# Performance work log

Hardware: AMD Instinct MI355X
Metric: run time of the kernel (lower is better)

The kernel has to match this reference:

```python
import jax, jax.numpy as jnp
import numpy as np

EMBED = 1024
HEADS = 16
HEAD_DIM = EMBED // HEADS
DIVIDER = int(np.sqrt(HEAD_DIM))  # torch code uses int(sqrt(head_dim)) == 8


def setup_inputs() -> dict:
    key = jax.random.key(0)
    ks = jax.random.split(key, 9)
    B, S = 2, 2048
    scale = 1.0 / np.sqrt(EMBED)
    def lin(kw, kb):
        W = jax.random.uniform(kw, (EMBED, EMBED), jnp.float32, -scale, scale)
        b = jax.random.uniform(kb, (EMBED,), jnp.float32, -scale, scale)
        return W, b
    Wq, bq = lin(ks[0], ks[1])
    Wk, bk = lin(ks[2], ks[3])
    Wv, bv = lin(ks[4], ks[5])
    Wo, bo = lin(ks[6], ks[7])
    x = jax.random.normal(ks[8], (B, S, EMBED), jnp.float32)
    return {"x": x, "Wq": Wq, "bq": bq, "Wk": Wk, "bk": bk,
            "Wv": Wv, "bv": bv, "Wo": Wo, "bo": bo}


def reference(x, Wq, bq, Wk, bk, Wv, bv, Wo, bo):
    B, S, _ = x.shape
    # projections (torch Linear: x @ W.T + b)
    q = x @ Wq.T + bq
    k = x @ Wk.T + bk
    v = x @ Wv.T + bv
    # split heads: [B, S, H, D] -> [B, H, S, D]
    def heads(t):
        return t.reshape(B, S, HEADS, HEAD_DIM).transpose(0, 2, 1, 3)
    q, k, v = heads(q), heads(k), heads(v)
    # scores [B, H, S, S]
    scores = jnp.einsum('bhsd,bhtd->bhst', q, k) / DIVIDER
    attn = jax.nn.softmax(scores, axis=-1)
    out = jnp.einsum('bhst,bhtd->bhsd', attn, v)
    out = out.transpose(0, 2, 1, 3).reshape(B, S, EMBED)
    return out @ Wo.T + bo
```

## Files before the change

### kernel.cpp

```cpp
#include <hip/hip_runtime.h>
#include <hip/hip_bf16.h>
#include <stdint.h>

using bf16 = __hip_bfloat16;
typedef __attribute__((ext_vector_type(8))) short   short8;
typedef __attribute__((ext_vector_type(4))) float   floatx4;
typedef __attribute__((ext_vector_type(2))) unsigned int uint2v;

static __device__ __forceinline__ unsigned short f2bf(float f) {
    return __builtin_bit_cast(unsigned short, __float2bfloat16(f));
}

static __device__ __forceinline__ uint4 load8bf(const void* p, size_t e, int f) {
    if (!f) return *(const uint4*)((const ushort*)p + e);
    const float* fp = (const float*)p + e;
    float4 a = *(const float4*)fp;
    float4 b = *(const float4*)(fp + 4);
    union { uint4 u; unsigned short s[8]; } r;
    r.s[0] = f2bf(a.x); r.s[1] = f2bf(a.y); r.s[2] = f2bf(a.z); r.s[3] = f2bf(a.w);
    r.s[4] = f2bf(b.x); r.s[5] = f2bf(b.y); r.s[6] = f2bf(b.z); r.s[7] = f2bf(b.w);
    return r.u;
}
static __device__ __forceinline__ float loadScalar(const void* p, int i, int f) {
    return f ? ((const float*)p)[i] : __bfloat162float(((const bf16*)p)[i]);
}

#define GLL16(g, l)                                                          \
    __builtin_amdgcn_global_load_lds(                                        \
        (const __attribute__((address_space(1))) void*)(g),                  \
        (__attribute__((address_space(3))) void*)(l), 16, 0, 0)

__global__ void detect_dtype(const ushort* __restrict__ x, int* __restrict__ flag) {
    __shared__ int cnt;
    if (threadIdx.x == 0) cnt = 0;
    __syncthreads();
    unsigned short u = x[threadIdx.x * 2];
    int e = (u >> 7) & 0xFF;
    int bad = (e > 133 || e < 94) ? 1 : 0;
    atomicAdd(&cnt, bad);
    __syncthreads();
    if (threadIdx.x == 0) *flag = (cnt > 64) ? 1 : 0;
}

__global__ void cvt_bf16(const void* __restrict__ x,  const void* __restrict__ Wq,
                         const void* __restrict__ Wk, const void* __restrict__ Wv,
                         const void* __restrict__ Wo,
                         ushort* __restrict__ out, const int* __restrict__ flagp)
{
    const int f = *flagp;
    const size_t M1 = (size_t)1 << 20, M4 = (size_t)4 << 20;
    size_t i = ((size_t)blockIdx.x * 256 + threadIdx.x) * 8;
    const void* src; size_t off;
    if (i < M4)            { src = x;  off = i; }
    else if (i < M4 + M1)  { src = Wq; off = i - M4; }
    else if (i < M4 + 2*M1){ src = Wk; off = i - (M4 + M1); }
    else if (i < M4 + 3*M1){ src = Wv; off = i - (M4 + 2*M1); }
    else                   { src = Wo; off = i - (M4 + 3*M1); }
    *(uint4*)(out + i) = load8bf(src, off, f);
}

__global__ __launch_bounds__(512, 4)
void gemm_dual(const ushort* __restrict__ A,
               const ushort* __restrict__ Wa, const ushort* __restrict__ Wb2,
               const void* __restrict__ Ba, const void* __restrict__ Bb,
               void* __restrict__ Oa, void* __restrict__ Ob_,
               int pa, int pb, int nb_off, int out_ext,
               const int* __restrict__ flagp)
{
    __shared__ ushort pool[32768];

    const int f  = *flagp;
    const int m0 = blockIdx.x * 128;
    const int n0a = blockIdx.y * 64;
    const int n0b = n0a + nb_off;
    const int tid  = threadIdx.x;
    const int lane = tid & 63;
    const int wave = tid >> 6;
    const int wm   = wave & 3;
    const int wn   = wave >> 2;
    const int r15  = lane & 15;
    const int quad = lane >> 4;

    const int   my_pm = wn ? pb : pa;
    const void* my_Bi = wn ? Bb : Ba;
    void*       my_O  = wn ? Ob_ : Oa;
    const int   my_n0 = wn ? n0b : n0a;

    const int l8 = lane >> 3, s8 = lane & 7;
    const int ar0 = wave * 16 + l8;
    const int ar1 = ar0 + 8;
    const int wr0 = wave * 16 + l8;
    const int wr1 = wr0 + 8;
    const ushort* gA0 = A + (size_t)(m0 + ar0) * 1024 + ((s8 ^ (ar0 & 7)) << 3);
    const ushort* gA1 = A + (size_t)(m0 + ar1) * 1024 + ((s8 ^ (ar1 & 7)) << 3);
    const ushort* gW0 = (wr0 < 64 ? Wa + (size_t)(n0a + wr0) * 1024
                                  : Wb2 + (size_t)(n0b + wr0 - 64) * 1024)
                        + ((s8 ^ (wr0 & 7)) << 3);
    const ushort* gW1 = (wr1 < 64 ? Wa + (size_t)(n0a + wr1) * 1024
                                  : Wb2 + (size_t)(n0b + wr1 - 64) * 1024)
                        + ((s8 ^ (wr1 & 7)) << 3);

    floatx4 acc[2][4];
#pragma unroll
    for (int mb = 0; mb < 2; mb++)
#pragma unroll
        for (int db = 0; db < 4; db++) acc[mb][db] = (floatx4){0.f, 0.f, 0.f, 0.f};

    GLL16(gA0, pool + wave * 1024);
    GLL16(gA1, pool + wave * 1024 + 512);
    GLL16(gW0, pool + 16384 + wave * 1024);
    GLL16(gW1, pool + 16384 + wave * 1024 + 512);

    for (int kb = 0; kb < 1024; kb += 64) {
        const int cur = (kb >> 6) & 1;
        ushort* xs  = pool + cur * 8192;
        ushort* wsm = pool + 16384 + cur * 8192;
        if (kb + 64 < 1024) {
            ushort* xn = pool + (cur ^ 1) * 8192;
            ushort* wn_ = pool + 16384 + (cur ^ 1) * 8192;
            GLL16(gA0 + kb + 64, xn + wave * 1024);
            GLL16(gA1 + kb + 64, xn + wave * 1024 + 512);
            GLL16(gW0 + kb + 64, wn_ + wave * 1024);
            GLL16(gW1 + kb + 64, wn_ + wave * 1024 + 512);
            asm volatile("s_waitcnt vmcnt(4)" ::: "memory");
        } else {
            asm volatile("s_waitcnt vmcnt(0)" ::: "memory");
        }
        __builtin_amdgcn_s_barrier();
        __builtin_amdgcn_sched_barrier(0);
#pragma unroll
        for (int ks = 0; ks < 2; ks++) {
            short8 af[2];
#pragma unroll
            for (int mb = 0; mb < 2; mb++) {
                int arow = wm * 32 + mb * 16 + r15;
                af[mb] = *(const short8*)(
                    &xs[arow * 64 + (((ks * 4 + quad) ^ (arow & 7)) << 3)]);
            }
#pragma unroll
            for (int db = 0; db < 4; db++) {
                int brow = wn * 64 + db * 16 + r15;
                short8 bv = *(const short8*)(
                    &wsm[brow * 64 + (((ks * 4 + quad) ^ (brow & 7)) << 3)]);
#pragma unroll
                for (int mb = 0; mb < 2; mb++)
                    acc[mb][db] = __builtin_amdgcn_mfma_f32_16x16x32_bf16(
                        af[mb], bv, acc[mb][db], 0, 0, 0);
            }
        }
        __builtin_amdgcn_s_barrier();
    }

    if (my_pm == 2) {
#pragma unroll
        for (int mb = 0; mb < 2; mb++)
#pragma unroll
            for (int db = 0; db < 4; db++) {
                int d = db * 16 + r15;
                float bias = loadScalar(my_Bi, my_n0 + d, f);
                int s4 = wm * 32 + mb * 16 + quad * 4;
                union { uint2 u; ushort us[4]; } pk;
#pragma unroll
                for (int r = 0; r < 4; r++) pk.us[r] = f2bf(acc[mb][db][r] + bias);
                *(uint2*)(&pool[d * 128 + (((s4 >> 3) ^ (d & 15)) << 3) + (s4 & 7)])
                    = pk.u;
            }
    } else {
#pragma unroll
        for (int mb = 0; mb < 2; mb++)
#pragma unroll
            for (int db = 0; db < 4; db++) {
                int col = my_n0 + db * 16 + r15;
                float bias = loadScalar(my_Bi, col, f);
#pragma unroll
                for (int r = 0; r < 4; r++) {
                    int row = m0 + wm * 32 + mb * 16 + quad * 4 + r;
                    float v = acc[mb][db][r] + bias;
                    if (my_pm == 1) {
                        int hh = col >> 6, d = col & 63;
                        int b_ = row >> 11, s = row & 2047;
                        ((ushort*)my_O)[(((size_t)(b_ * 16 + hh) * 2048 + s) << 6) + d]
                            = f2bf(v);
                    } else if (out_ext && f) {
                        ((float*)my_O)[(size_t)row * 1024 + col] = v;
                    } else {
                        ((ushort*)my_O)[(size_t)row * 1024 + col] = f2bf(v);
                    }
                }
            }
    }

    if (pa == 2 || pb == 2) {
        __syncthreads();
        void* OutT = (pb == 2) ? Ob_ : Oa;
        const int nT  = (pb == 2) ? n0b : n0a;
        const int b_  = m0 >> 11;
        const int h   = nT >> 6;
        const int sl0 = m0 & 2047;
#pragma unroll
        for (int rr = 0; rr < 2; rr++) {
            int idx = rr * 512 + tid;
            int d = idx >> 4, sgrp = idx & 15;
            uint4 v = *(const uint4*)(&pool[d * 128 + ((sgrp ^ (d & 15)) << 3)]);
            *(uint4*)((ushort*)OutT +
                      ((size_t)((b_ * 16 + h) * 64 + d) << 11) + sl0 + sgrp * 8) = v;
        }
    }
}

template<int BM>
__global__ __launch_bounds__(512, 4)
void gemm_bt(const void* __restrict__ A,
             const void* __restrict__ Wa, const void* __restrict__ Wb,
             const void* __restrict__ Ba, const void* __restrict__ Bb,
             void* __restrict__ Oa, void* __restrict__ Ob_,
             int pa, int pb, int a_ext, int out_ext,
             const int* __restrict__ flagp)
{
    constexpr int MB = BM / 128;
    constexpr int P  = BM / 64;
    constexpr int SG = BM / 8;
    __shared__ ushort pool[BM * 64 + 4096];

    const int f  = *flagp;
    const int fA = a_ext ? f : 0;
    const int z  = blockIdx.z;
    const void* W   = z ? Wb : Wa;
    const void* Bi  = z ? Bb : Ba;
    void*       Out = z ? Ob_ : Oa;
    const int   pm  = z ? pb : pa;

    const int m0 = blockIdx.x * BM;
    const int n0 = blockIdx.y * 64;
    const int tid  = threadIdx.x;
    const int lane = tid & 63;
    const int wave = tid >> 6;
    const int r15  = lane & 15;
    const int quad = lane >> 4;

    const int srow = tid >> 3;
    const int sg   = tid & 7;

    ushort* xs  = pool;
    ushort* wsm = pool + BM * 64;

    floatx4 acc[MB][4];
#pragma unroll
    for (int mb = 0; mb < MB; mb++)
#pragma unroll
        for (int db = 0; db < 4; db++) acc[mb][db] = (floatx4){0.f, 0.f, 0.f, 0.f};

    uint4 apre[P], wpre;
#pragma unroll
    for (int p = 0; p < P; p++)
        apre[p] = load8bf(A, (size_t)(m0 + srow + p * 64) * 1024 + sg * 8, fA);
    wpre = load8bf(W, (size_t)(n0 + srow) * 1024 + sg * 8, f);

    for (int kb = 0; kb < 1024; kb += 64) {
#pragma unroll
        for (int p = 0; p < P; p++) {
            int row = srow + p * 64;
            *(uint4*)(&xs[row * 64 + ((sg ^ (row & 7)) << 3)]) = apre[p];
        }
        *(uint4*)(&wsm[srow * 64 + ((sg ^ (srow & 7)) << 3)]) = wpre;
        __syncthreads();
        if (kb + 64 < 1024) {
#pragma unroll
            for (int p = 0; p < P; p++)
                apre[p] = load8bf(A, (size_t)(m0 + srow + p * 64) * 1024
                                      + kb + 64 + sg * 8, fA);
            wpre = load8bf(W, (size_t)(n0 + srow) * 1024 + kb + 64 + sg * 8, f);
        }
#pragma unroll
        for (int ks = 0; ks < 2; ks++) {
            short8 af[MB];
#pragma unroll
            for (int mb = 0; mb < MB; mb++) {
                int arow = wave * (16 * MB) + mb * 16 + r15;
                af[mb] = *(const short8*)(
                    &xs[arow * 64 + (((ks * 4 + quad) ^ (arow & 7)) << 3)]);
            }
#pragma unroll
            for (int db = 0; db < 4; db++) {
                int brow = db * 16 + r15;
                short8 bv = *(const short8*)(
                    &wsm[brow * 64 + (((ks * 4 + quad) ^ (brow & 7)) << 3)]);
#pragma unroll
                for (int mb = 0; mb < MB; mb++)
                    acc[mb][db] = __builtin_amdgcn_mfma_f32_16x16x32_bf16(
                        af[mb], bv, acc[mb][db], 0, 0, 0);
            }
        }
        __syncthreads();
    }

    if (pm == 2) {
#pragma unroll
        for (int mb = 0; mb < MB; mb++)
#pragma unroll
            for (int db = 0; db < 4; db++) {
                int d = db * 16 + r15;
                float bias = loadScalar(Bi, n0 + d, f);
                int s4 = wave * (16 * MB) + mb * 16 + quad * 4;
                union { uint2 u; ushort us[4]; } pk;
#pragma unroll
                for (int r = 0; r < 4; r++) pk.us[r] = f2bf(acc[mb][db][r] + bias);
                *(uint2*)(&pool[d * BM + (((s4 >> 3) ^ (d & 15)) << 3) + (s4 & 7)])
                    = pk.u;
            }
        __syncthreads();
        const int b_  = m0 >> 11;
        const int h   = n0 >> 6;
        const int sl0 = m0 & 2047;
#pragma unroll
        for (int rr = 0; rr < (64 * SG) / 512; rr++) {
            int idx = rr * 512 + tid;
            int d = idx / SG, sgrp = idx % SG;
            uint4 v = *(const uint4*)(&pool[d * BM + ((sgrp ^ (d & 15)) << 3)]);
            *(uint4*)((ushort*)Out +
                      ((size_t)((b_ * 16 + h) * 64 + d) << 11) + sl0 + sgrp * 8) = v;
        }
        return;
    }

#pragma unroll
    for (int mb = 0; mb < MB; mb++)
#pragma unroll
        for (int db = 0; db < 4; db++) {
            int col = n0 + db * 16 + r15;
            float bias = loadScalar(Bi, col, f);
#pragma unroll
            for (int r = 0; r < 4; r++) {
                int row = m0 + wave * (16 * MB) + mb * 16 + quad * 4 + r;
                float v = acc[mb][db][r] + bias;
                if (pm == 1) {
                    int hh = col >> 6, d = col & 63;
                    int b_ = row >> 11, s = row & 2047;
                    ((ushort*)Out)[(((size_t)(b_ * 16 + hh) * 2048 + s) << 6) + d]
                        = f2bf(v);
                } else if (out_ext && f) {
                    ((float*)Out)[(size_t)row * 1024 + col] = v;
                } else {
                    ((ushort*)Out)[(size_t)row * 1024 + col] = f2bf(v);
                }
            }
        }
}

__global__ __launch_bounds__(512, 4)
void attn_fused(const void* __restrict__ x, const void* __restrict__ Wq,
                const void* __restrict__ bq,
                const ushort* __restrict__ K, const ushort* __restrict__ VT,
                ushort* __restrict__ AO, const int* __restrict__ flagp,
                int xisbf)
{
    __shared__ ushort pool[24576];

    const int f   = *flagp;
    const int fx  = xisbf ? 0 : f;
    const int bh  = blockIdx.x;
    const int h   = bh & 15, b_ = bh >> 4;
    const int q0  = blockIdx.y * 128;
    const int tid  = threadIdx.x;
    const int lane = tid & 63;
    const int wave = tid >> 6;
    const int qg   = wave >> 1;
    const int kh   = wave & 1;
    const int r15  = lane & 15;
    const int quad = lane >> 4;
    const size_t base = (size_t)bh << 17;

    const int srow = tid >> 3;
    const int sg   = tid & 7;

    uint4 kpre = *(const uint4*)(K  + base + (size_t)srow * 64   + sg * 8);
    uint4 vpre = *(const uint4*)(VT + base + (size_t)srow * 2048 + sg * 8);

    floatx4 qacc[4];
#pragma unroll
    for (int db = 0; db < 4; db++) qacc[db] = (floatx4){0.f,0.f,0.f,0.f};

    uint4 xpre[2], wpre;
#pragma unroll
    for (int p = 0; p < 2; p++)
        xpre[p] = load8bf(x, (size_t)(b_ * 2048 + q0 + srow + p * 64) * 1024
                              + sg * 8, fx);
    wpre = load8bf(Wq, (size_t)(h * 64 + srow) * 1024 + sg * 8, fx);

    for (int kb = 0; kb < 1024; kb += 64) {
        int buf = (kb >> 6) & 1;
        ushort* xs  = pool + buf * 8192;
        ushort* wsm = pool + 16384 + buf * 4096;
#pragma unroll
        for (int p = 0; p < 2; p++) {
            int row = srow + p * 64;
            *(uint4*)(&xs[row * 64 + ((sg ^ (row & 7)) << 3)]) = xpre[p];
        }
        *(uint4*)(&wsm[srow * 64 + ((sg ^ (srow & 7)) << 3)]) = wpre;
        __syncthreads();
        if (kb + 64 < 1024) {
#pragma unroll
            for (int p = 0; p < 2; p++)
                xpre[p] = load8bf(x, (size_t)(b_ * 2048 + q0 + srow + p * 64) * 1024
                                      + kb + 64 + sg * 8, fx);
            wpre = load8bf(Wq, (size_t)(h * 64 + srow) * 1024 + kb + 64 + sg * 8, fx);
        }
#pragma unroll
        for (int ks = 0; ks < 2; ks++) {
            int arow = wave * 16 + r15;
            short8 af = *(const short8*)(
                &xs[arow * 64 + (((ks * 4 + quad) ^ (arow & 7)) << 3)]);
#pragma unroll
            for (int db = 0; db < 4; db++) {
                int brow = db * 16 + r15;
                short8 bv = *(const short8*)(
                    &wsm[brow * 64 + (((ks * 4 + quad) ^ (brow & 7)) << 3)]);
                qacc[db] = __builtin_amdgcn_mfma_f32_16x16x32_bf16(
                    af, bv, qacc[db], 0, 0, 0);
            }
        }
    }

    ushort* Qs = pool;
    const float csc = 0.1803368801f;
#pragma unroll
    for (int db = 0; db < 4; db++) {
        int d = db * 16 + r15;
        float bias = loadScalar(bq, h * 64 + d, f);
#pragma unroll
        for (int r = 0; r < 4; r++) {
            int q = wave * 16 + quad * 4 + r;
            Qs[q * 64 + (((d >> 3) ^ (q & 7)) << 3) + (d & 7)] =
                f2bf((qacc[db][r] + bias) * csc);
        }
    }
    __syncthreads();
    short8 qf2[2][2];
#pragma unroll
    for (int qb = 0; qb < 2; qb++)
#pragma unroll
        for (int ks = 0; ks < 2; ks++) {
            int arow = qg * 32 + qb * 16 + r15;
            qf2[qb][ks] = *(const short8*)(
                &Qs[arow * 64 + (((ks * 4 + quad) ^ (arow & 7)) << 3)]);
        }
    __syncthreads();

    floatx4 oacc[2][4], lacc[2];
#pragma unroll
    for (int qb = 0; qb < 2; qb++) {
#pragma unroll
        for (int db = 0; db < 4; db++) oacc[qb][db] = (floatx4){0.f,0.f,0.f,0.f};
        lacc[qb] = (floatx4){0.f,0.f,0.f,0.f};
    }
    short8 ones;
#pragma unroll
    for (int j = 0; j < 8; j++) ones[j] = (short)0x3F80;

    for (int t0 = 0; t0 < 2048; t0 += 64) {
        int buf = (t0 >> 6) & 1;
        ushort* Ks = pool + buf * 4096;
        ushort* Vt = pool + 8192 + buf * 4096;
        *(uint4*)(&Ks[srow * 64 + ((sg ^ (srow & 7)) << 3)]) = kpre;
        *(uint4*)(&Vt[srow * 64 + ((sg ^ (srow & 7)) << 3)]) = vpre;
        __syncthreads();
        if (t0 < 1984) {
            kpre = *(const uint4*)(K  + base + (size_t)(t0 + 64 + srow) * 64
                                       + sg * 8);
            vpre = *(const uint4*)(VT + base + (size_t)srow * 2048
                                       + t0 + 64 + sg * 8);
        }

        floatx4 s[2][2];
#pragma unroll
        for (int mb = 0; mb < 2; mb++)
#pragma unroll
            for (int qb = 0; qb < 2; qb++) s[mb][qb] = (floatx4){0.f,0.f,0.f,0.f};
#pragma unroll
        for (int ks = 0; ks < 2; ks++)
#pragma unroll
            for (int mb = 0; mb < 2; mb++) {
                int arow = kh * 32 + mb * 16 + r15;
                short8 kf = *(const short8*)(
                    &Ks[arow * 64 + (((ks * 4 + quad) ^ (arow & 7)) << 3)]);
#pragma unroll
                for (int qb = 0; qb < 2; qb++)
                    s[mb][qb] = __builtin_amdgcn_mfma_f32_16x16x32_bf16(
                        kf, qf2[qb][ks], s[mb][qb], 0, 0, 0);
            }

        uint Lr[2][2], Hr[2][2];
#pragma unroll
        for (int mb = 0; mb < 2; mb++)
#pragma unroll
            for (int qb = 0; qb < 2; qb++) {
                uint b0 = __builtin_bit_cast(uint, __builtin_amdgcn_exp2f(s[mb][qb][0]));
                uint b1 = __builtin_bit_cast(uint, __builtin_amdgcn_exp2f(s[mb][qb][1]));
                uint b2 = __builtin_bit_cast(uint, __builtin_amdgcn_exp2f(s[mb][qb][2]));
                uint b3 = __builtin_bit_cast(uint, __builtin_amdgcn_exp2f(s[mb][qb][3]));
                Lr[mb][qb] = (b1 & 0xFFFF0000u) | (b0 >> 16);
                Hr[mb][qb] = (b3 & 0xFFFF0000u) | (b2 >> 16);
            }
        short8 pf[2];
#pragma unroll
        for (int qb = 0; qb < 2; qb++) {
            uint2v tL = __builtin_amdgcn_permlane32_swap(
                Lr[0][qb], Lr[1][qb], false, false);
            uint2v uL = __builtin_amdgcn_permlane16_swap(
                tL[0], tL[1], false, false);
            uint2v tH = __builtin_amdgcn_permlane32_swap(
                Hr[0][qb], Hr[1][qb], false, false);
            uint2v uH = __builtin_amdgcn_permlane16_swap(
                tH[0], tH[1], false, false);
            union { uint u[4]; short8 s8; } pk;
            pk.u[0] = uL[0]; pk.u[1] = uH[0]; pk.u[2] = uL[1]; pk.u[3] = uH[1];
            pf[qb] = pk.s8;
        }

#pragma unroll
        for (int db = 0; db < 4; db++) {
            int brow = db * 16 + r15;
            short8 vf = *(const short8*)(
                &Vt[brow * 64 + (((kh * 4 + quad) ^ (brow & 7)) << 3)]);
#pragma unroll
            for (int qb = 0; qb < 2; qb++)
                oacc[qb][db] = __builtin_amdgcn_mfma_f32_16x16x32_bf16(
                    pf[qb], vf, oacc[qb][db], 0, 0, 0);
        }
#pragma unroll
        for (int qb = 0; qb < 2; qb++)
            lacc[qb] = __builtin_amdgcn_mfma_f32_16x16x32_bf16(
                pf[qb], ones, lacc[qb], 0, 0, 0);
    }

    __syncthreads();
    {
        char* rb = (char*)pool + qg * 10240 + lane * 16;
        if (kh) {
#pragma unroll
            for (int qb = 0; qb < 2; qb++) {
#pragma unroll
                for (int db = 0; db < 4; db++)
                    *(floatx4*)(rb + (qb * 4 + db) * 1024) = oacc[qb][db];
                *(floatx4*)(rb + (8 + qb) * 1024) = lacc[qb];
            }
        }
        __syncthreads();
        if (!kh) {
#pragma unroll
            for (int qb = 0; qb < 2; qb++) {
#pragma unroll
                for (int db = 0; db < 4; db++)
                    oacc[qb][db] += *(const floatx4*)(rb + (qb * 4 + db) * 1024);
                lacc[qb] += *(const floatx4*)(rb + (8 + qb) * 1024);
            }
            float inv[2][4];
#pragma unroll
            for (int qb = 0; qb < 2; qb++)
#pragma unroll
                for (int r = 0; r < 4; r++) inv[qb][r] = 1.f / lacc[qb][r];
#pragma unroll
            for (int qb = 0; qb < 2; qb++)
#pragma unroll
                for (int db = 0; db < 4; db++) {
                    int d = db * 16 + r15;
#pragma unroll
                    for (int r = 0; r < 4; r++) {
                        int qi = q0 + qg * 32 + qb * 16 + quad * 4 + r;
                        AO[((size_t)(b_ * 2048 + qi) << 10) + h * 64 + d] =
                            f2bf(oacc[qb][db][r] * inv[qb][r]);
                    }
                }
        }
    }
}

__global__ void copy_u4(const uint4* __restrict__ src, uint4* __restrict__ dst) {
    size_t i = (size_t)blockIdx.x * 256 + threadIdx.x;
    dst[i] = src[i];
}

extern "C" void kernel_launch(void* const* d_in, const int* in_sizes, int n_in,
                              void* d_out, int out_size, void* d_ws, size_t ws_size,
                              hipStream_t stream)
{
    const void* x  = d_in[0];
    const void* Wq = d_in[1];
    const void* bq = d_in[2];
    const void* Wk = d_in[3];
    const void* bk = d_in[4];
    const void* Wv = d_in[5];
    const void* bv = d_in[6];
    const void* Wo = d_in[7];
    const void* bo = d_in[8];

    const size_t TEN = (size_t)2 * 16 * 2048 * 64;
    const size_t M1  = (size_t)1 << 20;
    int*    flagp = (int*)d_ws;
    ushort* Kw    = (ushort*)((char*)d_ws + 256);
    ushort* Vw    = Kw + TEN;

    const size_t need_cvt = 256 + (2 * TEN + 8 * M1) * sizeof(ushort);
    const size_t need_aow = need_cvt + TEN * sizeof(ushort);

    detect_dtype<<<1, 256, 0, stream>>>((const ushort*)x, flagp);

    if (ws_size >= need_cvt) {
        ushort* CV  = Vw + TEN;
        ushort* xb  = CV;
        ushort* wqb = CV + 4 * M1;
        ushort* wkb = CV + 5 * M1;
        ushort* wvb = CV + 6 * M1;
        ushort* wob = CV + 7 * M1;
        const bool aow_ws = ws_size >= need_aow;
        ushort* AOw = aow_ws ? (CV + 8 * M1) : (ushort*)d_out;
        ushort* Oin = aow_ws ? AOw : Kw;

        cvt_bf16<<<dim3(4096), dim3(256), 0, stream>>>(
            x, Wq, Wk, Wv, Wo, CV, flagp);

        gemm_dual<<<dim3(32, 16), dim3(512), 0, stream>>>(
            xb, wkb, wvb, bk, bv, Kw, Vw, 1, 2,
            0, 0, flagp);

        attn_fused<<<dim3(32, 16), dim3(512), 0, stream>>>(
            xb, wqb, bq, Kw, Vw, AOw, flagp, 1);

        if (!aow_ws)
            copy_u4<<<dim3(2048), dim3(256), 0, stream>>>(
                (const uint4*)d_out, (uint4*)Oin);

        gemm_dual<<<dim3(32, 8), dim3(512), 0, stream>>>(
            Oin, wob, wob, bo, bo, d_out, d_out, 0, 0,
            512, 1, flagp);
    } else {
        const bool big_ws = ws_size >= 3 * TEN * sizeof(ushort) + 256;
        ushort* AOw = big_ws ? (Vw + TEN) : (ushort*)d_out;
        ushort* Oin = big_ws ? AOw : Kw;

        gemm_bt<128><<<dim3(32, 16, 2), dim3(512), 0, stream>>>(
            x, Wk, Wv, bk, bv, Kw, Vw, 1, 2, 1, 0, flagp);
        attn_fused<<<dim3(32, 16), dim3(512), 0, stream>>>(
            x, Wq, bq, Kw, Vw, AOw, flagp, 0);
        if (!big_ws)
            copy_u4<<<dim3(2048), dim3(256), 0, stream>>>(
                (const uint4*)d_out, (uint4*)Oin);
        gemm_bt<128><<<dim3(32, 16, 1), dim3(512), 0, stream>>>(
            Oin, Wo, Wo, bo, bo, d_out, d_out, 0, 0, 0, 1, flagp);
    }
}
```

Measured before the change: 198.8 us.

## Stream K/V tiles directly to LDS with async global loads and wave priority

Replaces the register-staged K/V prefetch in the attention loop with direct global-to-LDS loads (GLL16) into the alternate double-buffer, using explicit vmcnt waits and raw s_barrier. It also raises wave priority around the MFMA sections with s_setprio. The aim is to drop the register round-trip and the LDS store instructions, and to overlap the next tile's fetch with compute. It adds a second barrier per iteration and relies on the swizzled global address mapping matching the LDS layout; the initial tile is still written through registers.

New measurement: 206.9 us. +4.0%, slower.

```diff
diff --git a/kernel.cpp b/kernel.cpp
--- a/kernel.cpp
+++ b/kernel.cpp
@@ -457,25 +457,39 @@
 #pragma unroll
     for (int j = 0; j < 8; j++) ones[j] = (short)0x3F80;
 
-    for (int t0 = 0; t0 < 2048; t0 += 64) {
-        int buf = (t0 >> 6) & 1;
-        ushort* Ks = pool + buf * 4096;
-        ushort* Vt = pool + 8192 + buf * 4096;
-        *(uint4*)(&Ks[srow * 64 + ((sg ^ (srow & 7)) << 3)]) = kpre;
-        *(uint4*)(&Vt[srow * 64 + ((sg ^ (srow & 7)) << 3)]) = vpre;
-        __syncthreads();
-        if (t0 < 1984) {
-            kpre = *(const uint4*)(K  + base + (size_t)(t0 + 64 + srow) * 64
-                                       + sg * 8);
-            vpre = *(const uint4*)(VT + base + (size_t)srow * 2048
-                                       + t0 + 64 + sg * 8);
-        }
+    *(uint4*)(&pool[srow * 64 + ((sg ^ (srow & 7)) << 3)]) = kpre;
+    *(uint4*)(&pool[8192 + srow * 64 + ((sg ^ (srow & 7)) << 3)]) = vpre;
+
+    const int l8 = lane >> 3, s8 = lane & 7;
+    const int sgrow = wave * 8 + l8;
+    const ushort* gK = K  + base + (size_t)sgrow * 64   + ((s8 ^ l8) << 3);
+    const ushort* gV = VT + base + (size_t)sgrow * 2048 + ((s8 ^ l8) << 3);
+
+    for (int t = 0; t < 32; ++t) {
+        const int cur = t & 1;
+        ushort* Ks = pool + cur * 4096;
+        ushort* Vt = pool + 8192 + cur * 4096;
+        if (t < 31) {
+            ushort* Ksn = pool + (cur ^ 1) * 4096;
+            ushort* Vtn = pool + 8192 + (cur ^ 1) * 4096;
+            GLL16(gK + (size_t)(t + 1) * 4096, Ksn + wave * 512);
+            GLL16(gV + (t + 1) * 64,           Vtn + wave * 512);
+            if (t == 0)
+                asm volatile("s_waitcnt lgkmcnt(0)" ::: "memory");
+            else
+                asm volatile("s_waitcnt vmcnt(2)" ::: "memory");
+        } else {
+            asm volatile("s_waitcnt vmcnt(0)" ::: "memory");
+        }
+        __builtin_amdgcn_s_barrier();
+        __builtin_amdgcn_sched_barrier(0);
 
         floatx4 s[2][2];
 #pragma unroll
         for (int mb = 0; mb < 2; mb++)
 #pragma unroll
             for (int qb = 0; qb < 2; qb++) s[mb][qb] = (floatx4){0.f,0.f,0.f,0.f};
+        __builtin_amdgcn_s_setprio(1);
 #pragma unroll
         for (int ks = 0; ks < 2; ks++)
 #pragma unroll
@@ -488,6 +502,7 @@
                     s[mb][qb] = __builtin_amdgcn_mfma_f32_16x16x32_bf16(
                         kf, qf2[qb][ks], s[mb][qb], 0, 0, 0);
             }
+        __builtin_amdgcn_s_setprio(0);
 
         uint Lr[2][2], Hr[2][2];
 #pragma unroll
@@ -512,11 +527,12 @@
                 Hr[0][qb], Hr[1][qb], false, false);
             uint2v uH = __builtin_amdgcn_permlane16_swap(
                 tH[0], tH[1], false, false);
-            union { uint u[4]; short8 s8; } pk;
+            union { uint u[4]; short8 s8v; } pk;
             pk.u[0] = uL[0]; pk.u[1] = uH[0]; pk.u[2] = uL[1]; pk.u[3] = uH[1];
-            pf[qb] = pk.s8;
-        }
-
+            pf[qb] = pk.s8v;
+        }
+
+        __builtin_amdgcn_s_setprio(1);
 #pragma unroll
         for (int db = 0; db < 4; db++) {
             int brow = db * 16 + r15;
@@ -531,6 +547,9 @@
         for (int qb = 0; qb < 2; qb++)
             lacc[qb] = __builtin_amdgcn_mfma_f32_16x16x32_bf16(
                 pf[qb], ones, lacc[qb], 0, 0, 0);
+        __builtin_amdgcn_s_setprio(0);
+
+        __builtin_amdgcn_s_barrier();
     }
 
     __syncthreads();
```
